# Kernel optimization log

Hardware: AMD Instinct MI355X
Metric: run time of the kernel (lower is better)

The kernel has to match this reference:

```python
import jax, jax.numpy as jnp
import numpy as np

NEG_INF = -2.0**32 + 1.0  # matches torch paddings value


def prelu(x, a):
    return jnp.where(x >= 0, x, a * x)


def setup_inputs() -> dict:
    key = jax.random.key(0)
    ks = jax.random.split(key, 12)
    B, L, D, A = 2048, 200, 128, 64
    return {
        "query": jax.random.normal(ks[0], (B, D), jnp.float32),
        "keys": jax.random.normal(ks[1], (B, L, D), jnp.float32),
        "keys_length": jax.random.randint(ks[2], (B,), 0, L, jnp.int64 if jax.config.jax_enable_x64 else jnp.int32),
        "W1": jax.random.normal(ks[3], (4 * D, A), jnp.float32) * (1.0 / np.sqrt(4 * D)),
        "b1": jax.random.normal(ks[4], (A,), jnp.float32) * 0.01,
        "a1": jnp.full((1,), 0.25, jnp.float32),  # PReLU default init
        "W2": jax.random.normal(ks[5], (A, A), jnp.float32) * (1.0 / np.sqrt(A)),
        "b2": jax.random.normal(ks[6], (A,), jnp.float32) * 0.01,
        "a2": jnp.full((1,), 0.25, jnp.float32),
        "W3": jax.random.normal(ks[7], (A, 1), jnp.float32) * (1.0 / np.sqrt(A)),
        "b3": jax.random.normal(ks[8], (1,), jnp.float32) * 0.01,
    }


def reference(query, keys, keys_length, W1, b1, a1, W2, b2, a2, W3, b3):
    B, L, D = keys.shape
    q = jnp.broadcast_to(query[:, None, :], (B, L, D))
    # concat features: [q, k, q-k, q*k] -> (B, L, 4D)
    q_k = jnp.concatenate([q, keys, q - keys, q * keys], axis=-1)
    h = prelu(jnp.einsum("blf,fa->bla", q_k, W1) + b1, a1)
    h = prelu(jnp.einsum("bla,ac->blc", h, W2) + b2, a2)
    scores = (jnp.einsum("bla,ao->blo", h, W3) + b3)[..., 0]  # (B, L)
    mask = jnp.arange(L)[None, :] < keys_length[:, None]
    scores = jnp.where(mask, scores, NEG_INF)
    att = jax.nn.softmax(scores, axis=1)
    out = jnp.einsum("bl,bld->bd", att, keys)  # bmm(att[:,None,:], keys)
    return out, att
```

## Files before the change

### kernel.cpp

```cpp
#include <hip/hip_runtime.h>
#include <math.h>

typedef __attribute__((ext_vector_type(8))) _Float16 half8;
typedef __attribute__((ext_vector_type(4))) float float4_t;

#define NB 2048
#define LL 200
#define DD 128
#define AA 64
#define NEG_INF_F -4294967295.0f

#define WQ_STRIDE 136

#define WS_WBC_H  0
#define WS_W1D_H  8704
#define WS_W2T_H  17408
#define WS_QA_OFF 43008

__global__ __launch_bounds__(256)
void din_prep(const float* __restrict__ query,
              const float* __restrict__ W1,
              const float* __restrict__ b1,
              const float* __restrict__ W2,
              _Float16* __restrict__ ws16,
              float* __restrict__ qa)
{
    const int tid = threadIdx.x;
    const int blk = blockIdx.x;

    if (blk < 128) {
        __shared__ float sW1s[DD * AA];
        __shared__ float sq[16 * DD];
        const int b0 = blk * 16;
        for (int i = tid; i < DD * AA; i += 256)
            sW1s[i] = W1[i] + W1[2 * DD * AA + i];
        for (int i = tid; i < 16 * DD; i += 256)
            sq[i] = query[(size_t)b0 * DD + i];
        __syncthreads();
        const int lane = tid & 63, bb = tid >> 6;
        for (int g = 0; g < 4; ++g) {
            const int bi = bb * 4 + g;
            float acc = b1[lane];
            #pragma unroll 8
            for (int d = 0; d < DD; ++d)
                acc += sq[bi * DD + d] * sW1s[d * AA + lane];
            qa[(size_t)(b0 + bi) * AA + lane] = acc;
        }
    } else if (blk == 128) {
        for (int i = tid; i < 64 * 17; i += 256) {
            const int a = i / 17, c = i - a * 17;
            half8 hb, hd;
            if (c == 16) {
                #pragma unroll
                for (int j = 0; j < 8; ++j) { hb[j] = (_Float16)0.f; hd[j] = (_Float16)0.f; }
            } else {
                const int d0 = c * 8;
                #pragma unroll
                for (int j = 0; j < 8; ++j) {
                    const int d = d0 + j;
                    hb[j] = (_Float16)(W1[(DD + d) * AA + a] - W1[(2 * DD + d) * AA + a]);
                    hd[j] = (_Float16)(W1[(3 * DD + d) * AA + a]);
                }
            }
            *(half8*)&ws16[WS_WBC_H + a * WQ_STRIDE + c * 8] = hb;
            *(half8*)&ws16[WS_W1D_H + a * WQ_STRIDE + c * 8] = hd;
        }
    } else {
        _Float16* w2t = ws16 + WS_W2T_H;
        const int c = tid >> 2, j0 = (tid & 3) * 16;
        for (int ch = 0; ch < 2; ++ch) {
            half8 v;
            #pragma unroll
            for (int j = 0; j < 8; ++j)
                v[j] = (_Float16)W2[(j0 + ch * 8 + j) * AA + c];
            *(half8*)&w2t[c * AA + j0 + ch * 8] = v;
        }
    }
}

__global__ __launch_bounds__(256, 2)
void din_main(const float* __restrict__ keys,
              const int*   __restrict__ keys_length,
              const float* __restrict__ a1p,
              const float* __restrict__ b2,
              const float* __restrict__ a2p,
              const float* __restrict__ W3,
              const _Float16* __restrict__ ws16,
              const float* __restrict__ qa,
              const float* __restrict__ query,
              float* __restrict__ out,
              float* __restrict__ att)
{
    __shared__ __align__(16) _Float16 sKeys[LL * DD];
    __shared__ __align__(16) _Float16 sWq[AA * WQ_STRIDE];
    __shared__ __align__(16) _Float16 sH1[4 * 16 * 72];
    __shared__ float sQ[136];
    __shared__ float sS[224];
    __shared__ float sRed[16];

    const int tid  = threadIdx.x;
    const int lane = tid & 63, wv = tid >> 6;
    const int col  = lane & 15, quad = lane >> 4;
    const int b    = blockIdx.x;
    const int len  = keys_length[b];
    const float pa1 = a1p[0], pa2 = a2p[0];
    const int Lcap = (len == 0) ? LL : len;

    if (tid < 136) sQ[tid] = (tid < 128) ? query[(size_t)b * DD + tid] : 0.f;
    for (int i = tid; i < 224; i += 256) sS[i] = NEG_INF_F;
    __syncthreads();

    for (int ci = tid; ci < 64 * 17; ci += 256) {
        const int c = ci % 17;
        const int d0 = c * 8;
        const half8 hb = *(const half8*)&ws16[WS_WBC_H + ci * 8];
        const half8 hd = *(const half8*)&ws16[WS_W1D_H + ci * 8];
        half8 r;
        #pragma unroll
        for (int j = 0; j < 8; ++j)
            r[j] = (_Float16)((float)hb[j] + sQ[d0 + j] * (float)hd[j]);
        *(half8*)&sWq[ci * 8] = r;
    }
    for (int i = tid; i < Lcap * 16; i += 256) {
        const int l = i >> 4, c8 = i & 15;
        const float* kp = keys + ((size_t)b * LL + l) * DD + c8 * 8;
        const float4 v0 = *(const float4*)kp;
        const float4 v1 = *(const float4*)(kp + 4);
        half8 h;
        h[0] = (_Float16)v0.x; h[1] = (_Float16)v0.y; h[2] = (_Float16)v0.z; h[3] = (_Float16)v0.w;
        h[4] = (_Float16)v1.x; h[5] = (_Float16)v1.y; h[6] = (_Float16)v1.z; h[7] = (_Float16)v1.w;
        *(half8*)&sKeys[l * DD + ((c8 ^ (l & 7)) << 3)] = h;
    }
    __syncthreads();

    const _Float16* w2t = ws16 + WS_W2T_H;
    half8 w2f[2][4];
    #pragma unroll
    for (int ks = 0; ks < 2; ++ks)
        #pragma unroll
        for (int n = 0; n < 4; ++n)
            w2f[ks][n] = *(const half8*)&w2t[(n * 16 + col) * AA + ks * 32 + quad * 8];
    float qareg[4], b2reg[4], w3reg[4];
    #pragma unroll
    for (int n = 0; n < 4; ++n) {
        qareg[n] = qa[(size_t)b * AA + n * 16 + col];
        b2reg[n] = b2[n * 16 + col];
        w3reg[n] = W3[n * 16 + col];
    }

    const int ntiles = (len + 15) >> 4;
    _Float16* const myH = &sH1[wv * 16 * 72];

    for (int t = wv; t < ntiles; t += 4) {
        const int l0 = t * 16;
        const int lr = (l0 + col < LL) ? (l0 + col) : (LL - 1);

        float4_t C[4] = {{0,0,0,0},{0,0,0,0},{0,0,0,0},{0,0,0,0}};
        #pragma unroll
        for (int ks = 0; ks < 4; ++ks) {
            const int swz = ((ks * 4 + quad) ^ (lr & 7)) << 3;
            const half8 af = *(const half8*)&sKeys[lr * DD + swz];
            const int ko = ks * 32 + quad * 8;
            #pragma unroll
            for (int n = 0; n < 4; ++n) {
                const half8 bf = *(const half8*)&sWq[(n * 16 + col) * WQ_STRIDE + ko];
                C[n] = __builtin_amdgcn_mfma_f32_16x16x32_f16(af, bf, C[n], 0, 0, 0);
            }
        }
        #pragma unroll
        for (int n = 0; n < 4; ++n)
            #pragma unroll
            for (int r = 0; r < 4; ++r) {
                float v = C[n][r] + qareg[n];
                v = v >= 0.f ? v : pa1 * v;
                myH[(quad * 4 + r) * 72 + n * 16 + col] = (_Float16)v;
            }
        float4_t D[4] = {{0,0,0,0},{0,0,0,0},{0,0,0,0},{0,0,0,0}};
        #pragma unroll
        for (int ks = 0; ks < 2; ++ks) {
            const half8 af = *(const half8*)&myH[col * 72 + ks * 32 + quad * 8];
            #pragma unroll
            for (int n = 0; n < 4; ++n)
                D[n] = __builtin_amdgcn_mfma_f32_16x16x32_f16(af, w2f[ks][n], D[n], 0, 0, 0);
        }
        float pr[4] = {0.f, 0.f, 0.f, 0.f};
        #pragma unroll
        for (int n = 0; n < 4; ++n)
            #pragma unroll
            for (int r = 0; r < 4; ++r) {
                float v = D[n][r] + b2reg[n];
                v = v >= 0.f ? v : pa2 * v;
                pr[r] += v * w3reg[n];
            }
        #pragma unroll
        for (int r = 0; r < 4; ++r) {
            float pv = pr[r];
            pv += __shfl_xor(pv, 1);
            pv += __shfl_xor(pv, 2);
            pv += __shfl_xor(pv, 4);
            pv += __shfl_xor(pv, 8);
            const int l = l0 + quad * 4 + r;
            if (col == 0 && l < len) sS[l] = pv;
        }
    }

    __syncthreads();
    float m = (tid < LL) ? sS[tid] : -INFINITY;
    #pragma unroll
    for (int o = 1; o < 64; o <<= 1) m = fmaxf(m, __shfl_xor(m, o));
    if (lane == 0) sRed[wv] = m;
    __syncthreads();
    const float M = fmaxf(fmaxf(sRed[0], sRed[1]), fmaxf(sRed[2], sRed[3]));
    float e = (tid < LL) ? expf(sS[tid] - M) : 0.f;
    float s = e;
    #pragma unroll
    for (int o = 1; o < 64; o <<= 1) s += __shfl_xor(s, o);
    if (lane == 0) sRed[8 + wv] = s;
    __syncthreads();
    const float S = sRed[8] + sRed[9] + sRed[10] + sRed[11];
    const float inv = 1.f / S;
    if (tid < LL) {
        const float v = e * inv;
        sS[tid] = v;
        att[(size_t)b * LL + tid] = v;
    }
    __syncthreads();

    {
        const int c8 = tid & 15, ph = tid >> 4;
        float acc[8];
        #pragma unroll
        for (int j = 0; j < 8; ++j) acc[j] = 0.f;
        for (int l = ph; l < Lcap; l += 16) {
            const float w = sS[l];
            const half8 kv = *(const half8*)&sKeys[l * DD + ((c8 ^ (l & 7)) << 3)];
            #pragma unroll
            for (int j = 0; j < 8; ++j) acc[j] += w * (float)kv[j];
        }
        float* const scratch = (float*)sWq;
        #pragma unroll
        for (int j = 0; j < 8; ++j) scratch[tid * 8 + j] = acc[j];
        __syncthreads();
        if (tid < DD) {
            const int c8o = tid >> 3, j = tid & 7;
            float r = 0.f;
            #pragma unroll
            for (int p = 0; p < 16; ++p) r += scratch[(p * 16 + c8o) * 8 + j];
            out[(size_t)b * DD + tid] = r;
        }
    }
}

extern "C" void kernel_launch(void* const* d_in, const int* in_sizes, int n_in,
                              void* d_out, int out_size, void* d_ws, size_t ws_size,
                              hipStream_t stream) {
    (void)in_sizes; (void)n_in; (void)ws_size; (void)out_size;
    const float* query = (const float*)d_in[0];
    const float* keys  = (const float*)d_in[1];
    const int*   klen  = (const int*)d_in[2];
    const float* W1    = (const float*)d_in[3];
    const float* b1    = (const float*)d_in[4];
    const float* a1    = (const float*)d_in[5];
    const float* W2    = (const float*)d_in[6];
    const float* b2    = (const float*)d_in[7];
    const float* a2    = (const float*)d_in[8];
    const float* W3    = (const float*)d_in[9];

    _Float16* ws16 = (_Float16*)d_ws;
    float*    qawk = (float*)((char*)d_ws + WS_QA_OFF);

    float* out = (float*)d_out;
    float* att = out + (size_t)NB * DD;

    hipLaunchKernelGGL(din_prep, dim3(130), dim3(256), 0, stream,
                       query, W1, b1, W2, ws16, qawk);
    hipLaunchKernelGGL(din_main, dim3(NB), dim3(256), 0, stream,
                       keys, klen, a1, b2, a2, W3, ws16, qawk, query, out, att);
}
```

Baseline: 325.6 us.

## Stream key tiles per wave with online softmax instead of staging all keys

Before, each block staged all of a batch row's keys in LDS as fp16, about 51 KB. Now each wave loads its own 16-row key tile, runs the MLP on it, and accumulates the attention-weighted key sum with a running-max (flash-style) online softmax. Per-wave partial sums are merged at the end using the global max. This cuts LDS use enough to raise the occupancy target to three blocks per SM. It also drops the separate pass over keys for the output, and rows with zero length get a fallback that computes a uniform mean. The cost is extra exp and rescale work per tile, plus global loads that are no longer all issued up front.

```diff
diff --git a/kernel.cpp b/kernel.cpp
--- a/kernel.cpp
+++ b/kernel.cpp
@@ -78,7 +78,7 @@
     }
 }
 
-__global__ __launch_bounds__(256, 2)
+__global__ __launch_bounds__(256, 3)
 void din_main(const float* __restrict__ keys,
               const int*   __restrict__ keys_length,
               const float* __restrict__ a1p,
@@ -91,11 +91,12 @@
               float* __restrict__ out,
               float* __restrict__ att)
 {
-    __shared__ __align__(16) _Float16 sKeys[LL * DD];
     __shared__ __align__(16) _Float16 sWq[AA * WQ_STRIDE];
+    __shared__ __align__(16) _Float16 sTile[4 * 16 * DD];
     __shared__ __align__(16) _Float16 sH1[4 * 16 * 72];
     __shared__ float sQ[136];
     __shared__ float sS[224];
+    __shared__ float sML[16];
     __shared__ float sRed[16];
 
     const int tid  = threadIdx.x;
@@ -104,7 +105,6 @@
     const int b    = blockIdx.x;
     const int len  = keys_length[b];
     const float pa1 = a1p[0], pa2 = a2p[0];
-    const int Lcap = (len == 0) ? LL : len;
 
     if (tid < 136) sQ[tid] = (tid < 128) ? query[(size_t)b * DD + tid] : 0.f;
     for (int i = tid; i < 224; i += 256) sS[i] = NEG_INF_F;
@@ -121,16 +121,6 @@
             r[j] = (_Float16)((float)hb[j] + sQ[d0 + j] * (float)hd[j]);
         *(half8*)&sWq[ci * 8] = r;
     }
-    for (int i = tid; i < Lcap * 16; i += 256) {
-        const int l = i >> 4, c8 = i & 15;
-        const float* kp = keys + ((size_t)b * LL + l) * DD + c8 * 8;
-        const float4 v0 = *(const float4*)kp;
-        const float4 v1 = *(const float4*)(kp + 4);
-        half8 h;
-        h[0] = (_Float16)v0.x; h[1] = (_Float16)v0.y; h[2] = (_Float16)v0.z; h[3] = (_Float16)v0.w;
-        h[4] = (_Float16)v1.x; h[5] = (_Float16)v1.y; h[6] = (_Float16)v1.z; h[7] = (_Float16)v1.w;
-        *(half8*)&sKeys[l * DD + ((c8 ^ (l & 7)) << 3)] = h;
-    }
     __syncthreads();
 
     const _Float16* w2t = ws16 + WS_W2T_H;
@@ -149,17 +139,36 @@
     }
 
     const int ntiles = (len + 15) >> 4;
-    _Float16* const myH = &sH1[wv * 16 * 72];
+    _Float16* const myTile = &sTile[wv * 16 * DD];
+    _Float16* const myH    = &sH1[wv * 16 * 72];
+
+    float m_run = -INFINITY;
+    float O[8];
+    #pragma unroll
+    for (int j = 0; j < 8; ++j) O[j] = 0.f;
 
     for (int t = wv; t < ntiles; t += 4) {
         const int l0 = t * 16;
-        const int lr = (l0 + col < LL) ? (l0 + col) : (LL - 1);
+
+        #pragma unroll
+        for (int it = 0; it < 4; ++it) {
+            const int i = lane + 64 * it;
+            const int row = i >> 4, c8 = i & 15;
+            const int l = l0 + row;
+            const int lr = (l < LL) ? l : (LL - 1);
+            const float* kp = keys + ((size_t)b * LL + lr) * DD + c8 * 8;
+            const float4 v0 = *(const float4*)kp;
+            const float4 v1 = *(const float4*)(kp + 4);
+            half8 h;
+            h[0] = (_Float16)v0.x; h[1] = (_Float16)v0.y; h[2] = (_Float16)v0.z; h[3] = (_Float16)v0.w;
+            h[4] = (_Float16)v1.x; h[5] = (_Float16)v1.y; h[6] = (_Float16)v1.z; h[7] = (_Float16)v1.w;
+            *(half8*)&myTile[row * DD + ((c8 ^ (row & 7)) << 3)] = h;
+        }
 
         float4_t C[4] = {{0,0,0,0},{0,0,0,0},{0,0,0,0},{0,0,0,0}};
         #pragma unroll
         for (int ks = 0; ks < 4; ++ks) {
-            const int swz = ((ks * 4 + quad) ^ (lr & 7)) << 3;
-            const half8 af = *(const half8*)&sKeys[lr * DD + swz];
+            const half8 af = *(const half8*)&myTile[col * DD + (((ks * 4 + quad) ^ (col & 7)) << 3)];
             const int ko = ks * 32 + quad * 8;
             #pragma unroll
             for (int n = 0; n < 4; ++n) {
@@ -192,6 +201,7 @@
                 v = v >= 0.f ? v : pa2 * v;
                 pr[r] += v * w3reg[n];
             }
+        float sv[4];
         #pragma unroll
         for (int r = 0; r < 4; ++r) {
             float pv = pr[r];
@@ -200,11 +210,34 @@
             pv += __shfl_xor(pv, 4);
             pv += __shfl_xor(pv, 8);
             const int l = l0 + quad * 4 + r;
-            if (col == 0 && l < len) sS[l] = pv;
-        }
-    }
-
-    __syncthreads();
+            const bool valid = (l < len);
+            sv[r] = valid ? pv : -INFINITY;
+            if (col == 0 && valid) sS[l] = pv;
+        }
+        const float tmax = fmaxf(fmaxf(sv[0], sv[1]), fmaxf(sv[2], sv[3]));
+        const float newm = fmaxf(m_run, tmax);
+        if (newm != -INFINITY) {
+            const float alpha = expf(m_run - newm);
+            #pragma unroll
+            for (int j = 0; j < 8; ++j) O[j] *= alpha;
+            #pragma unroll
+            for (int r = 0; r < 4; ++r) {
+                const float e = (sv[r] == -INFINITY) ? 0.f : expf(sv[r] - newm);
+                const int rr = quad * 4 + r;
+                const half8 kv = *(const half8*)&myTile[rr * DD + ((col ^ (rr & 7)) << 3)];
+                #pragma unroll
+                for (int j = 0; j < 8; ++j) O[j] += e * (float)kv[j];
+            }
+            m_run = newm;
+        }
+    }
+
+    float* const myO = (float*)myH;
+    #pragma unroll
+    for (int j = 0; j < 8; ++j) myO[quad * 128 + col * 8 + j] = O[j];
+    if (col == 0) sML[wv * 4 + quad] = m_run;
+    __syncthreads();
+
     float m = (tid < LL) ? sS[tid] : -INFINITY;
     #pragma unroll
     for (int o = 1; o < 64; o <<= 1) m = fmaxf(m, __shfl_xor(m, o));
@@ -219,35 +252,32 @@
     __syncthreads();
     const float S = sRed[8] + sRed[9] + sRed[10] + sRed[11];
     const float inv = 1.f / S;
-    if (tid < LL) {
-        const float v = e * inv;
-        sS[tid] = v;
-        att[(size_t)b * LL + tid] = v;
-    }
-    __syncthreads();
-
-    {
-        const int c8 = tid & 15, ph = tid >> 4;
-        float acc[8];
-        #pragma unroll
-        for (int j = 0; j < 8; ++j) acc[j] = 0.f;
-        for (int l = ph; l < Lcap; l += 16) {
-            const float w = sS[l];
-            const half8 kv = *(const half8*)&sKeys[l * DD + ((c8 ^ (l & 7)) << 3)];
-            #pragma unroll
-            for (int j = 0; j < 8; ++j) acc[j] += w * (float)kv[j];
-        }
-        float* const scratch = (float*)sWq;
-        #pragma unroll
-        for (int j = 0; j < 8; ++j) scratch[tid * 8 + j] = acc[j];
+    if (tid < LL) att[(size_t)b * LL + tid] = e * inv;
+
+    if (tid < 16) sML[tid] = expf(sML[tid] - M);
+    __syncthreads();
+
+    if (len > 0) {
+        if (tid < DD) {
+            const float* fO = (const float*)sH1;
+            float r = 0.f;
+            #pragma unroll
+            for (int w = 0; w < 4; ++w)
+                #pragma unroll
+                for (int q = 0; q < 4; ++q)
+                    r += sML[w * 4 + q] * fO[w * 576 + q * 128 + tid];
+            out[(size_t)b * DD + tid] = r * inv;
+        }
+    } else {
+        const int d = tid & 127, ph = tid >> 7;
+        float acc = 0.f;
+        for (int l = ph; l < LL; l += 2)
+            acc += keys[((size_t)b * LL + l) * DD + d];
+        float* const sc = (float*)sTile;
+        sc[tid] = acc;
         __syncthreads();
-        if (tid < DD) {
-            const int c8o = tid >> 3, j = tid & 7;
-            float r = 0.f;
-            #pragma unroll
-            for (int p = 0; p < 16; ++p) r += scratch[(p * 16 + c8o) * 8 + j];
-            out[(size_t)b * DD + tid] = r;
-        }
+        if (tid < DD)
+            out[(size_t)b * DD + tid] = (sc[tid] + sc[tid + 128]) * (1.f / 200.f);
     }
 }
 
```

Result: slower. 361.5 us (+11.0%).

## Hold query-scaled W1 fragments in registers and batch key loads

Applied to the files above, without the earlier changes.

The query-dependent W1 operand for the first MFMA layer is now built directly into per-lane registers. This removes the shared-memory staging buffer, a barrier, and the LDS reads inside the tile loop. Key rows are loaded in two unrolled batches of global float4 loads into registers before the fp16 conversion and swizzled LDS stores, so more loads are in flight at once. The prep kernel is also split across more blocks, each handling 4 queries instead of 16. The cost is higher VGPR pressure from the 64 operand registers plus 52 staged float4 values, which risks spills or lower occupancy.

```diff
diff --git a/kernel.cpp b/kernel.cpp
--- a/kernel.cpp
+++ b/kernel.cpp
@@ -28,25 +28,22 @@
     const int tid = threadIdx.x;
     const int blk = blockIdx.x;
 
-    if (blk < 128) {
+    if (blk < 512) {
         __shared__ float sW1s[DD * AA];
-        __shared__ float sq[16 * DD];
-        const int b0 = blk * 16;
+        __shared__ float sq[4 * DD];
+        const int b0 = blk * 4;
         for (int i = tid; i < DD * AA; i += 256)
             sW1s[i] = W1[i] + W1[2 * DD * AA + i];
-        for (int i = tid; i < 16 * DD; i += 256)
+        for (int i = tid; i < 4 * DD; i += 256)
             sq[i] = query[(size_t)b0 * DD + i];
         __syncthreads();
-        const int lane = tid & 63, bb = tid >> 6;
-        for (int g = 0; g < 4; ++g) {
-            const int bi = bb * 4 + g;
-            float acc = b1[lane];
-            #pragma unroll 8
-            for (int d = 0; d < DD; ++d)
-                acc += sq[bi * DD + d] * sW1s[d * AA + lane];
-            qa[(size_t)(b0 + bi) * AA + lane] = acc;
-        }
-    } else if (blk == 128) {
+        const int lane = tid & 63, bi = tid >> 6;
+        float acc = b1[lane];
+        #pragma unroll 8
+        for (int d = 0; d < DD; ++d)
+            acc += sq[bi * DD + d] * sW1s[d * AA + lane];
+        qa[(size_t)(b0 + bi) * AA + lane] = acc;
+    } else if (blk == 512) {
         for (int i = tid; i < 64 * 17; i += 256) {
             const int a = i / 17, c = i - a * 17;
             half8 hb, hd;
@@ -92,9 +89,7 @@
               float* __restrict__ att)
 {
     __shared__ __align__(16) _Float16 sKeys[LL * DD];
-    __shared__ __align__(16) _Float16 sWq[AA * WQ_STRIDE];
     __shared__ __align__(16) _Float16 sH1[4 * 16 * 72];
-    __shared__ float sQ[136];
     __shared__ float sS[224];
     __shared__ float sRed[16];
 
@@ -106,33 +101,29 @@
     const float pa1 = a1p[0], pa2 = a2p[0];
     const int Lcap = (len == 0) ? LL : len;
 
-    if (tid < 136) sQ[tid] = (tid < 128) ? query[(size_t)b * DD + tid] : 0.f;
     for (int i = tid; i < 224; i += 256) sS[i] = NEG_INF_F;
-    __syncthreads();
-
-    for (int ci = tid; ci < 64 * 17; ci += 256) {
-        const int c = ci % 17;
-        const int d0 = c * 8;
-        const half8 hb = *(const half8*)&ws16[WS_WBC_H + ci * 8];
-        const half8 hd = *(const half8*)&ws16[WS_W1D_H + ci * 8];
-        half8 r;
-        #pragma unroll
-        for (int j = 0; j < 8; ++j)
-            r[j] = (_Float16)((float)hb[j] + sQ[d0 + j] * (float)hd[j]);
-        *(half8*)&sWq[ci * 8] = r;
-    }
-    for (int i = tid; i < Lcap * 16; i += 256) {
-        const int l = i >> 4, c8 = i & 15;
-        const float* kp = keys + ((size_t)b * LL + l) * DD + c8 * 8;
-        const float4 v0 = *(const float4*)kp;
-        const float4 v1 = *(const float4*)(kp + 4);
-        half8 h;
-        h[0] = (_Float16)v0.x; h[1] = (_Float16)v0.y; h[2] = (_Float16)v0.z; h[3] = (_Float16)v0.w;
-        h[4] = (_Float16)v1.x; h[5] = (_Float16)v1.y; h[6] = (_Float16)v1.z; h[7] = (_Float16)v1.w;
-        *(half8*)&sKeys[l * DD + ((c8 ^ (l & 7)) << 3)] = h;
-    }
-    __syncthreads();
-
+
+    half8 wqf[4][4];
+    #pragma unroll
+    for (int ks = 0; ks < 4; ++ks) {
+        const int d0 = ks * 32 + quad * 8;
+        const float4 q0 = *(const float4*)(query + (size_t)b * DD + d0);
+        const float4 q1 = *(const float4*)(query + (size_t)b * DD + d0 + 4);
+        float qv[8];
+        qv[0] = q0.x; qv[1] = q0.y; qv[2] = q0.z; qv[3] = q0.w;
+        qv[4] = q1.x; qv[5] = q1.y; qv[6] = q1.z; qv[7] = q1.w;
+        #pragma unroll
+        for (int n = 0; n < 4; ++n) {
+            const int a = n * 16 + col;
+            const half8 hb = *(const half8*)&ws16[WS_WBC_H + a * WQ_STRIDE + d0];
+            const half8 hd = *(const half8*)&ws16[WS_W1D_H + a * WQ_STRIDE + d0];
+            half8 r;
+            #pragma unroll
+            for (int j = 0; j < 8; ++j)
+                r[j] = (_Float16)((float)hb[j] + qv[j] * (float)hd[j]);
+            wqf[ks][n] = r;
+        }
+    }
     const _Float16* w2t = ws16 + WS_W2T_H;
     half8 w2f[2][4];
     #pragma unroll
@@ -148,6 +139,55 @@
         w3reg[n] = W3[n * 16 + col];
     }
 
+    const int NI = Lcap * 16;
+    {
+        float4 va[7], vb[7];
+        #pragma unroll
+        for (int it = 0; it < 7; ++it) {
+            const int i = tid + it * 256;
+            const int ii = (i < NI) ? i : (NI - 1);
+            const float* kp = keys + ((size_t)b * LL + (ii >> 4)) * DD + (ii & 15) * 8;
+            va[it] = *(const float4*)kp;
+            vb[it] = *(const float4*)(kp + 4);
+        }
+        #pragma unroll
+        for (int it = 0; it < 7; ++it) {
+            const int i = tid + it * 256;
+            if (i < NI) {
+                const int l = i >> 4, c8 = i & 15;
+                half8 h;
+                h[0] = (_Float16)va[it].x; h[1] = (_Float16)va[it].y;
+                h[2] = (_Float16)va[it].z; h[3] = (_Float16)va[it].w;
+                h[4] = (_Float16)vb[it].x; h[5] = (_Float16)vb[it].y;
+                h[6] = (_Float16)vb[it].z; h[7] = (_Float16)vb[it].w;
+                *(half8*)&sKeys[l * DD + ((c8 ^ (l & 7)) << 3)] = h;
+            }
+        }
+        float4 vc[6], vd[6];
+        #pragma unroll
+        for (int it = 0; it < 6; ++it) {
+            const int i = tid + (7 + it) * 256;
+            const int ii = (i < NI) ? i : (NI - 1);
+            const float* kp = keys + ((size_t)b * LL + (ii >> 4)) * DD + (ii & 15) * 8;
+            vc[it] = *(const float4*)kp;
+            vd[it] = *(const float4*)(kp + 4);
+        }
+        #pragma unroll
+        for (int it = 0; it < 6; ++it) {
+            const int i = tid + (7 + it) * 256;
+            if (i < NI) {
+                const int l = i >> 4, c8 = i & 15;
+                half8 h;
+                h[0] = (_Float16)vc[it].x; h[1] = (_Float16)vc[it].y;
+                h[2] = (_Float16)vc[it].z; h[3] = (_Float16)vc[it].w;
+                h[4] = (_Float16)vd[it].x; h[5] = (_Float16)vd[it].y;
+                h[6] = (_Float16)vd[it].z; h[7] = (_Float16)vd[it].w;
+                *(half8*)&sKeys[l * DD + ((c8 ^ (l & 7)) << 3)] = h;
+            }
+        }
+    }
+    __syncthreads();
+
     const int ntiles = (len + 15) >> 4;
     _Float16* const myH = &sH1[wv * 16 * 72];
 
@@ -158,14 +198,10 @@
         float4_t C[4] = {{0,0,0,0},{0,0,0,0},{0,0,0,0},{0,0,0,0}};
         #pragma unroll
         for (int ks = 0; ks < 4; ++ks) {
-            const int swz = ((ks * 4 + quad) ^ (lr & 7)) << 3;
-            const half8 af = *(const half8*)&sKeys[lr * DD + swz];
-            const int ko = ks * 32 + quad * 8;
-            #pragma unroll
-            for (int n = 0; n < 4; ++n) {
-                const half8 bf = *(const half8*)&sWq[(n * 16 + col) * WQ_STRIDE + ko];
-                C[n] = __builtin_amdgcn_mfma_f32_16x16x32_f16(af, bf, C[n], 0, 0, 0);
-            }
+            const half8 af = *(const half8*)&sKeys[lr * DD + (((ks * 4 + quad) ^ (lr & 7)) << 3)];
+            #pragma unroll
+            for (int n = 0; n < 4; ++n)
+                C[n] = __builtin_amdgcn_mfma_f32_16x16x32_f16(af, wqf[ks][n], C[n], 0, 0, 0);
         }
         #pragma unroll
         for (int n = 0; n < 4; ++n)
@@ -237,7 +273,7 @@
             #pragma unroll
             for (int j = 0; j < 8; ++j) acc[j] += w * (float)kv[j];
         }
-        float* const scratch = (float*)sWq;
+        float* const scratch = (float*)sH1;
         #pragma unroll
         for (int j = 0; j < 8; ++j) scratch[tid * 8 + j] = acc[j];
         __syncthreads();
@@ -272,7 +308,7 @@
     float* out = (float*)d_out;
     float* att = out + (size_t)NB * DD;
 
-    hipLaunchKernelGGL(din_prep, dim3(130), dim3(256), 0, stream,
+    hipLaunchKernelGGL(din_prep, dim3(514), dim3(256), 0, stream,
                        query, W1, b1, W2, ws16, qawk);
     hipLaunchKernelGGL(din_main, dim3(NB), dim3(256), 0, stream,
                        keys, klen, a1, b2, a2, W3, ws16, qawk, query, out, att);
```

New measurement: 329.8 us. No clear change (+1.3%).
